# Performance work log

Measured on AMD Instinct MI355X. Metric: run time of the kernel, lower is better.

Reference implementation:

```python
import jax, jax.numpy as jnp
import numpy as np

BN_EPS = 1e-5
MIN_DIST = 1e-10


def _conv_bn_relu(x, w, b, gamma, beta):
    # pointwise Conv1d (kernel=1) == per-point linear, then BatchNorm1d (training-mode
    # batch stats, biased variance, as torch does for normalization), then ReLU.
    y = jnp.einsum('oc,bcn->bon', w, x) + b[None, :, None]
    mu = y.mean(axis=(0, 2))
    var = y.var(axis=(0, 2))
    yn = (y - mu[None, :, None]) * jax.lax.rsqrt(var + BN_EPS)[None, :, None]
    return jax.nn.relu(yn * gamma[None, :, None] + beta[None, :, None])


def setup_inputs() -> dict:
    key = jax.random.key(0)
    ks = jax.random.split(key, 12)
    B, N1, N2, C1, C2 = 8, 8192, 2048, 128, 256
    in_ch = C1 + C2  # 384
    mlp = [256, 128]
    inp = {
        'xyz1': jax.random.normal(ks[0], (B, N1, 3), jnp.float32),
        'xyz2': jax.random.normal(ks[1], (B, N2, 3), jnp.float32),
        'points1': jax.random.normal(ks[2], (B, C1, N1), jnp.float32),
        'points2': jax.random.normal(ks[3], (B, C2, N2), jnp.float32),
    }
    last = in_ch
    for i, out_ch in enumerate(mlp):
        scale = 1.0 / np.sqrt(last)
        inp[f'w{i}'] = jax.random.uniform(ks[4 + 2 * i], (out_ch, last), jnp.float32, -scale, scale)
        inp[f'b{i}'] = jax.random.uniform(ks[5 + 2 * i], (out_ch,), jnp.float32, -scale, scale)
        inp[f'gamma{i}'] = jnp.ones((out_ch,), jnp.float32)
        inp[f'beta{i}'] = jnp.zeros((out_ch,), jnp.float32)
        last = out_ch
    return inp


def reference(xyz1, xyz2, points1, points2,
              w0, b0, gamma0, beta0, w1, b1, gamma1, beta1):
    # Euclidean distance matrix [B, N1, N2] (torch.cdist, p=2)
    sq = (jnp.sum(xyz1 * xyz1, -1)[:, :, None]
          + jnp.sum(xyz2 * xyz2, -1)[:, None, :]
          - 2.0 * jnp.einsum('bnd,bmd->bnm', xyz1, xyz2))
    dists = jnp.sqrt(jnp.maximum(sq, 0.0))
    # 3 smallest distances + indices (ascending, matching torch.topk largest=False)
    neg_d, knn_idx = jax.lax.top_k(-dists, 3)  # [B, N1, 3]
    knn_d = jnp.maximum(-neg_d, MIN_DIST)
    weights = 1.0 / knn_d
    weights = weights / jnp.sum(weights, axis=2, keepdims=True)  # [B, N1, 3]
    # gather neighbor features: points2 [B, C2, N2] -> [B, C2, N1, 3]
    knn_feats = jnp.take_along_axis(points2[:, :, None, :],
                                    knn_idx[:, None, :, :], axis=3)
    interpolated = jnp.sum(knn_feats * weights[:, None, :, :], axis=3)  # [B, C2, N1]
    new_points = jnp.concatenate([points1, interpolated], axis=1)  # [B, C1+C2, N1]
    new_points = _conv_bn_relu(new_points, w0, b0, gamma0, beta0)
    new_points = _conv_bn_relu(new_points, w1, b1, gamma1, beta1)
    return new_points
```

## Files before the change

kernel.cpp:

```cpp
#include <hip/hip_runtime.h>
#include <cstdint>

using u16 = unsigned short;
typedef short bf16x8 __attribute__((ext_vector_type(8)));
typedef float f32x4 __attribute__((ext_vector_type(4)));

__device__ __forceinline__ float bf2f(u16 h) {
    union { unsigned u; float f; } x;
    x.u = ((unsigned)h) << 16;
    return x.f;
}
__device__ __forceinline__ u16 f2bf(float f) {
    union { float f; unsigned u; } x;
    x.f = f;
    unsigned r = x.u + 0x7fffu + ((x.u >> 16) & 1u);
    return (u16)(r >> 16);
}

__device__ __forceinline__ void gl_lds16(const u16* g, u16* l) {
    __builtin_amdgcn_global_load_lds((const __attribute__((address_space(1))) void*)g,
                                     (__attribute__((address_space(3))) void*)l, 16, 0, 0);
}

#define N1 8192
#define N2 2048
#define C2 256

__global__ __launch_bounds__(256) void prep_misc(const float* __restrict__ w0,
                                                 const float* __restrict__ w1,
                                                 const float* __restrict__ xyz2,
                                                 u16* __restrict__ w0b,
                                                 u16* __restrict__ w1b,
                                                 float4* __restrict__ P2P,
                                                 float* __restrict__ stats) {
    int bid = blockIdx.x, tid = threadIdx.x;
    if (bid < 384) {
        int i = bid * 256 + tid;
        w0b[i] = f2bf(w0[i]);
    } else if (bid < 512) {
        int i = (bid - 384) * 256 + tid;
        w1b[i] = f2bf(w1[i]);
    } else if (bid < 576) {
        int i = (bid - 512) * 256 + tid;
        float x = xyz2[i * 3 + 0], y = xyz2[i * 3 + 1], z = xyz2[i * 3 + 2];
        float nsq = __fadd_rn(__fadd_rn(__fmul_rn(x, x), __fmul_rn(y, y)), __fmul_rn(z, z));
        P2P[i] = make_float4(-2.0f * x, -2.0f * y, -2.0f * z, nsq);
    } else {
        for (int i = tid; i < 768; i += 256) stats[i] = 0.0f;
    }
}

__global__ __launch_bounds__(256) void transpose_to_bf16(const float* __restrict__ src,
                                                         u16* __restrict__ dst,
                                                         int C, int N, int dst_stride,
                                                         int col_off) {
    __shared__ float tile[32][33];
    int b = blockIdx.z;
    int n0 = blockIdx.x * 32, c0 = blockIdx.y * 32;
    int tx = threadIdx.x & 31, ty = threadIdx.x >> 5;
    const float* s = src + (long)b * C * N;
#pragma unroll
    for (int i = 0; i < 4; i++) {
        int c = ty + i * 8;
        tile[c][tx] = s[(long)(c0 + c) * N + n0 + tx];
    }
    __syncthreads();
    u16* d = dst + (long)b * N * dst_stride;
#pragma unroll
    for (int i = 0; i < 4; i++) {
        int n = ty + i * 8;
        d[(long)(n0 + n) * dst_stride + col_off + c0 + tx] = f2bf(tile[tx][n]);
    }
}

__global__ __launch_bounds__(512) void knn_interp(const float* __restrict__ xyz1,
                                                  const float4* __restrict__ P2P,
                                                  const u16* __restrict__ P2T,
                                                  u16* __restrict__ X) {
    __shared__ float4 pts[N2];
    __shared__ float m_d[8][64][3];
    __shared__ int   m_i[8][64][3];
    __shared__ int   s_idx[64][3];
    __shared__ float s_w[64][3];
    int b = blockIdx.y;
    int n0 = blockIdx.x * 64;
    int tid = threadIdx.x;
    int ql = tid & 63;
    int part = __builtin_amdgcn_readfirstlane(tid >> 6);

    {
        const float4* src = P2P + (long)b * N2;
        for (int j = tid; j < N2; j += 512) pts[j] = src[j];
    }

    int n = n0 + ql;
    float px = xyz1[((long)b * N1 + n) * 3 + 0];
    float py = xyz1[((long)b * N1 + n) * 3 + 1];
    float pz = xyz1[((long)b * N1 + n) * 3 + 2];
    float psq = __fadd_rn(__fadd_rn(__fmul_rn(px, px), __fmul_rn(py, py)), __fmul_rn(pz, pz));
    __syncthreads();

    const float4* lp = &pts[part * (N2 / 8)];
    int jbase = part * (N2 / 8);
    float b0 = 1e30f, b1 = 1e30f, b2 = 1e30f;
    int i0 = 0, i1 = 0, i2 = 0;
#pragma unroll 8
    for (int jj = 0; jj < N2 / 8; jj++) {
        float4 p = lp[jj];
        float u = __fadd_rn(__fadd_rn(__fmul_rn(p.x, px), __fmul_rn(p.y, py)),
                            __fmul_rn(p.z, pz));
        float sq = __fadd_rn(__fadd_rn(psq, p.w), u);
        int j = jbase + jj;
        bool c0 = sq < b0, c1 = sq < b1, c2 = sq < b2;
        i2 = c2 ? (c1 ? i1 : j) : i2;
        i1 = c1 ? (c0 ? i0 : j) : i1;
        i0 = c0 ? j : i0;
        float m1 = fmaxf(b0, sq);
        b0 = fminf(b0, sq);
        float m2 = fmaxf(b1, m1);
        b1 = fminf(b1, m1);
        b2 = fminf(b2, m2);
    }
    m_d[part][ql][0] = b0; m_d[part][ql][1] = b1; m_d[part][ql][2] = b2;
    m_i[part][ql][0] = i0; m_i[part][ql][1] = i1; m_i[part][ql][2] = i2;
    __syncthreads();

    if (tid < 64) {
        float c0 = 1e30f, c1 = 1e30f, c2 = 1e30f;
        int a0 = 0x7fffffff, a1 = 0x7fffffff, a2 = 0x7fffffff;
#pragma unroll
        for (int pp2 = 0; pp2 < 8; pp2++) {
#pragma unroll
            for (int k = 0; k < 3; k++) {
                float d = m_d[pp2][tid][k];
                int ix = m_i[pp2][tid][k];
                if (d < c2 || (d == c2 && ix < a2)) {
                    if (d < c1 || (d == c1 && ix < a1)) {
                        c2 = c1; a2 = a1;
                        if (d < c0 || (d == c0 && ix < a0)) { c1 = c0; a1 = a0; c0 = d; a0 = ix; }
                        else                                { c1 = d; a1 = ix; }
                    } else { c2 = d; a2 = ix; }
                }
            }
        }
        float e0 = sqrtf(fmaxf(c0, 0.0f));
        float e1 = sqrtf(fmaxf(c1, 0.0f));
        float e2 = sqrtf(fmaxf(c2, 0.0f));
        float kd0 = fmaxf(e0, 1e-10f), kd1 = fmaxf(e1, 1e-10f), kd2 = fmaxf(e2, 1e-10f);
        float w0 = __fdiv_rn(1.0f, kd0), w1 = __fdiv_rn(1.0f, kd1), w2 = __fdiv_rn(1.0f, kd2);
        float wsum = __fadd_rn(__fadd_rn(w0, w1), w2);
        s_idx[tid][0] = a0; s_idx[tid][1] = a1; s_idx[tid][2] = a2;
        s_w[tid][0] = __fdiv_rn(w0, wsum);
        s_w[tid][1] = __fdiv_rn(w1, wsum);
        s_w[tid][2] = __fdiv_rn(w2, wsum);
    }
    __syncthreads();

    int l = tid & 63;
    const u16* base = P2T + (long)b * N2 * C2;
    for (int p = part; p < 64; p += 8) {
        int j0 = s_idx[p][0], j1 = s_idx[p][1], j2 = s_idx[p][2];
        float f0 = s_w[p][0], f1 = s_w[p][1], f2 = s_w[p][2];
        ushort4 r0 = *(const ushort4*)&base[(long)j0 * C2 + l * 4];
        ushort4 r1 = *(const ushort4*)&base[(long)j1 * C2 + l * 4];
        ushort4 r2 = *(const ushort4*)&base[(long)j2 * C2 + l * 4];
        ushort4 o;
        o.x = f2bf(__fadd_rn(__fadd_rn(__fmul_rn(bf2f(r0.x), f0), __fmul_rn(bf2f(r1.x), f1)),
                             __fmul_rn(bf2f(r2.x), f2)));
        o.y = f2bf(__fadd_rn(__fadd_rn(__fmul_rn(bf2f(r0.y), f0), __fmul_rn(bf2f(r1.y), f1)),
                             __fmul_rn(bf2f(r2.y), f2)));
        o.z = f2bf(__fadd_rn(__fadd_rn(__fmul_rn(bf2f(r0.z), f0), __fmul_rn(bf2f(r1.z), f1)),
                             __fmul_rn(bf2f(r2.z), f2)));
        o.w = f2bf(__fadd_rn(__fadd_rn(__fmul_rn(bf2f(r0.w), f0), __fmul_rn(bf2f(r1.w), f1)),
                             __fmul_rn(bf2f(r2.w), f2)));
        *(ushort4*)&X[(long)(b * N1 + n0 + p) * 384 + 128 + l * 4] = o;
    }
}

template <int KDIM, bool BN_IN, bool ASYNC>
__global__ __launch_bounds__(256) void gemm_bn(const u16* __restrict__ A,
                                               const u16* __restrict__ Bw,
                                               const float* __restrict__ bias,
                                               const float* __restrict__ g_in_sum,
                                               const float* __restrict__ g_in_ssq,
                                               const float* __restrict__ gamma_in,
                                               const float* __restrict__ beta_in,
                                               u16* __restrict__ Yout, int Ntot,
                                               float* __restrict__ g_out_sum,
                                               float* __restrict__ g_out_ssq) {
    constexpr int LD = ASYNC ? 32 : 40;
    __shared__ __align__(16) u16 Al[128 * LD];
    __shared__ __align__(16) u16 Bl[128 * LD];
    __shared__ float s_stats[256];
    __shared__ float s_scale[BN_IN ? KDIM : 2];
    __shared__ float s_shift[BN_IN ? KDIM : 2];

    int tid = threadIdx.x;
    long s0 = (long)blockIdx.x * 128;
    int o0 = blockIdx.y * 128;

    s_stats[tid] = 0.0f;
    if constexpr (BN_IN) {
        for (int k = tid; k < KDIM; k += 256) {
            float mu = g_in_sum[k] * (1.0f / 65536.0f);
            float var = g_in_ssq[k] * (1.0f / 65536.0f) - mu * mu;
            float rs = rsqrtf(var + 1e-5f);
            float sc = gamma_in[k] * rs;
            s_scale[k] = sc;
            s_shift[k] = beta_in[k] - mu * sc;
        }
    }
    int wid = tid >> 6, lane = tid & 63;
    int wm = wid >> 1, wn = wid & 1;
    int q = lane >> 4, l16 = lane & 15;

    f32x4 acc[4][4];
#pragma unroll
    for (int mi = 0; mi < 4; mi++)
#pragma unroll
        for (int ni = 0; ni < 4; ni++) acc[mi][ni] = (f32x4){0.f, 0.f, 0.f, 0.f};

    int rbase0 = wid * 32;
    int rsub = lane >> 2;
    int colsw = (((lane & 3) ^ (rsub & 3)) << 3);
    const u16* gA0 = A + (s0 + rbase0 + rsub) * KDIM + colsw;
    const u16* gA1 = gA0 + (long)16 * KDIM;
    const u16* gB0 = Bw + (long)(o0 + rbase0 + rsub) * KDIM + colsw;
    const u16* gB1 = gB0 + (long)16 * KDIM;
    u16* lA0 = &Al[rbase0 * 32];
    u16* lA1 = &Al[(rbase0 + 16) * 32];
    u16* lB0 = &Bl[rbase0 * 32];
    u16* lB1 = &Bl[(rbase0 + 16) * 32];
    int qA = ASYNC ? (q ^ (l16 & 3)) : q;

    __syncthreads();

    for (int kt = 0; kt < KDIM; kt += 32) {
        if constexpr (ASYNC) {
            gl_lds16(gA0 + kt, lA0);
            gl_lds16(gA1 + kt, lA1);
            gl_lds16(gB0 + kt, lB0);
            gl_lds16(gB1 + kt, lB1);
        } else {
#pragma unroll
            for (int cc = 0; cc < 2; cc++) {
                int ci = tid + cc * 256;
                int row = ci >> 2;
                int kc = (ci & 3) << 3;
                union { uint4 u; u16 h[8]; } va;
                va.u = *(const uint4*)(A + (s0 + row) * KDIM + kt + kc);
                if constexpr (BN_IN) {
#pragma unroll
                    for (int j = 0; j < 8; j++) {
                        float f = bf2f(va.h[j]);
                        f = fmaxf(fmaf(f, s_scale[kt + kc + j], s_shift[kt + kc + j]), 0.0f);
                        va.h[j] = f2bf(f);
                    }
                }
                *(uint4*)&Al[row * LD + kc] = va.u;
                *(uint4*)&Bl[row * LD + kc] = *(const uint4*)(Bw + (long)(o0 + row) * KDIM + kt + kc);
            }
        }
        __syncthreads();
        bf16x8 af[4], bfr[4];
#pragma unroll
        for (int mi = 0; mi < 4; mi++)
            af[mi] = *(const bf16x8*)&Al[(wm * 64 + mi * 16 + l16) * LD + qA * 8];
#pragma unroll
        for (int ni = 0; ni < 4; ni++)
            bfr[ni] = *(const bf16x8*)&Bl[(wn * 64 + ni * 16 + l16) * LD + qA * 8];
#pragma unroll
        for (int mi = 0; mi < 4; mi++)
#pragma unroll
            for (int ni = 0; ni < 4; ni++)
                acc[mi][ni] = __builtin_amdgcn_mfma_f32_16x16x32_bf16(af[mi], bfr[ni],
                                                                      acc[mi][ni], 0, 0, 0);
        __syncthreads();
    }

#pragma unroll
    for (int ni = 0; ni < 4; ni++) {
        int coll = wn * 64 + ni * 16 + l16;
        int col = o0 + coll;
        float bz = bias[col];
        float s1 = 0.0f, s2 = 0.0f;
#pragma unroll
        for (int mi = 0; mi < 4; mi++) {
#pragma unroll
            for (int r = 0; r < 4; r++) {
                float v = acc[mi][ni][r] + bz;
                s1 += v;
                s2 += v * v;
                long row = s0 + wm * 64 + mi * 16 + q * 4 + r;
                Yout[row * Ntot + col] = f2bf(v);
            }
        }
        s1 += __shfl_xor(s1, 16, 64);
        s1 += __shfl_xor(s1, 32, 64);
        s2 += __shfl_xor(s2, 16, 64);
        s2 += __shfl_xor(s2, 32, 64);
        if (q == 0) {
            atomicAdd(&s_stats[coll], s1);
            atomicAdd(&s_stats[128 + coll], s2);
        }
    }
    __syncthreads();
    if (tid < 128) {
        atomicAdd(&g_out_sum[o0 + tid], s_stats[tid]);
        atomicAdd(&g_out_ssq[o0 + tid], s_stats[128 + tid]);
    }
}

__global__ __launch_bounds__(256) void finalize_k(const u16* __restrict__ Y1,
                                                  const float* __restrict__ g_sum,
                                                  const float* __restrict__ g_ssq,
                                                  const float* __restrict__ gamma,
                                                  const float* __restrict__ beta,
                                                  float* __restrict__ out) {
    __shared__ float s_scale[128], s_shift[128];
    int tid = threadIdx.x;
    if (tid < 128) {
        float mu = g_sum[tid] * (1.0f / 65536.0f);
        float var = g_ssq[tid] * (1.0f / 65536.0f) - mu * mu;
        float rs = rsqrtf(var + 1e-5f);
        float sc = gamma[tid] * rs;
        s_scale[tid] = sc;
        s_shift[tid] = beta[tid] - mu * sc;
    }
    __syncthreads();
    long s = (long)blockIdx.x * 256 + tid;
    int b = (int)(s >> 13);
    int n = (int)(s & 8191);
    const u16* yrow = Y1 + s * 128;
    float* obase = out + (long)b * 128 * 8192 + n;
#pragma unroll
    for (int oc = 0; oc < 128; oc += 8) {
        union { uint4 u; u16 h[8]; } va;
        va.u = *(const uint4*)&yrow[oc];
#pragma unroll
        for (int k = 0; k < 8; k++) {
            int o = oc + k;
            float v = fmaxf(fmaf(bf2f(va.h[k]), s_scale[o], s_shift[o]), 0.0f);
            obase[(long)o * 8192] = v;
        }
    }
}

extern "C" void kernel_launch(void* const* d_in, const int* in_sizes, int n_in,
                              void* d_out, int out_size, void* d_ws, size_t ws_size,
                              hipStream_t stream) {
    const float* xyz1    = (const float*)d_in[0];
    const float* xyz2    = (const float*)d_in[1];
    const float* points1 = (const float*)d_in[2];
    const float* points2 = (const float*)d_in[3];
    const float* w0 = (const float*)d_in[4];
    const float* b0 = (const float*)d_in[5];
    const float* gamma0 = (const float*)d_in[6];
    const float* beta0 = (const float*)d_in[7];
    const float* w1 = (const float*)d_in[8];
    const float* b1 = (const float*)d_in[9];
    const float* gamma1 = (const float*)d_in[10];
    const float* beta1 = (const float*)d_in[11];
    float* out = (float*)d_out;

    char* ws = (char*)d_ws;
    u16* X      = (u16*)(ws + 0);
    u16* P2T    = (u16*)(ws + 50331648);
    u16* w0b    = (u16*)(ws + 58720256);
    u16* w1b    = (u16*)(ws + 58916864);
    u16* Y0     = (u16*)(ws + 58982400);
    float4* P2P = (float4*)(ws + 92536832);
    u16* Y1b    = (u16*)(ws + 92798976);
    float* stats = (float*)(ws + 126091264);
    if (ws_size < 126094336) return;
    float* gsum0 = stats;
    float* gss0  = stats + 256;
    float* gsum1 = stats + 512;
    float* gss1  = stats + 640;

    prep_misc<<<577, 256, 0, stream>>>(w0, w1, xyz2, w0b, w1b, P2P, stats);
    transpose_to_bf16<<<dim3(256, 4, 8), 256, 0, stream>>>(points1, X, 128, 8192, 384, 0);
    transpose_to_bf16<<<dim3(64, 8, 8), 256, 0, stream>>>(points2, P2T, 256, 2048, 256, 0);
    knn_interp<<<dim3(128, 8), 512, 0, stream>>>(xyz1, P2P, P2T, X);
    gemm_bn<384, false, true><<<dim3(512, 2), 256, 0, stream>>>(
        X, w0b, b0, nullptr, nullptr, nullptr, nullptr, Y0, 256, gsum0, gss0);
    gemm_bn<256, true, false><<<dim3(512, 1), 256, 0, stream>>>(
        Y0, w1b, b1, gsum0, gss0, gamma0, beta0, Y1b, 128, gsum1, gss1);
    finalize_k<<<256, 256, 0, stream>>>(Y1b, gsum1, gss1, gamma1, beta1, out);
}
```

Before: 277.6 us.

## Compute xyz2 norms inside knn kernel and halve threads per block

Drops the P2P precompute from prep_misc, so knn_interp now loads raw xyz2 and computes squared norms into LDS itself. The block shrinks from 512 to 256 threads, so each of 4 parts scans N2/4 candidates instead of 8 parts scanning N2/8. The branchless min/max top-3 update becomes a branchy insertion. The distance formula now computes -2*dot explicitly. The intent is to cut a precompute pass and workspace traffic, at the cost of less parallelism per query and possible wave divergence in the scan.

```diff
diff --git a/kernel.cpp b/kernel.cpp
--- a/kernel.cpp
+++ b/kernel.cpp
@@ -28,10 +28,8 @@
 
 __global__ __launch_bounds__(256) void prep_misc(const float* __restrict__ w0,
                                                  const float* __restrict__ w1,
-                                                 const float* __restrict__ xyz2,
                                                  u16* __restrict__ w0b,
                                                  u16* __restrict__ w1b,
-                                                 float4* __restrict__ P2P,
                                                  float* __restrict__ stats) {
     int bid = blockIdx.x, tid = threadIdx.x;
     if (bid < 384) {
@@ -40,11 +38,6 @@
     } else if (bid < 512) {
         int i = (bid - 384) * 256 + tid;
         w1b[i] = f2bf(w1[i]);
-    } else if (bid < 576) {
-        int i = (bid - 512) * 256 + tid;
-        float x = xyz2[i * 3 + 0], y = xyz2[i * 3 + 1], z = xyz2[i * 3 + 2];
-        float nsq = __fadd_rn(__fadd_rn(__fmul_rn(x, x), __fmul_rn(y, y)), __fmul_rn(z, z));
-        P2P[i] = make_float4(-2.0f * x, -2.0f * y, -2.0f * z, nsq);
     } else {
         for (int i = tid; i < 768; i += 256) stats[i] = 0.0f;
     }
@@ -73,53 +66,53 @@
     }
 }
 
-__global__ __launch_bounds__(512) void knn_interp(const float* __restrict__ xyz1,
-                                                  const float4* __restrict__ P2P,
+__global__ __launch_bounds__(256) void knn_interp(const float* __restrict__ xyz1,
+                                                  const float* __restrict__ xyz2,
                                                   const u16* __restrict__ P2T,
                                                   u16* __restrict__ X) {
     __shared__ float4 pts[N2];
-    __shared__ float m_d[8][64][3];
-    __shared__ int   m_i[8][64][3];
+    __shared__ float m_d[4][64][3];
+    __shared__ int   m_i[4][64][3];
     __shared__ int   s_idx[64][3];
     __shared__ float s_w[64][3];
     int b = blockIdx.y;
     int n0 = blockIdx.x * 64;
     int tid = threadIdx.x;
     int ql = tid & 63;
-    int part = __builtin_amdgcn_readfirstlane(tid >> 6);
-
-    {
-        const float4* src = P2P + (long)b * N2;
-        for (int j = tid; j < N2; j += 512) pts[j] = src[j];
-    }
+    int part = tid >> 6;
+
+    for (int j = tid; j < N2; j += 256) {
+        float x = xyz2[((long)b * N2 + j) * 3 + 0];
+        float y = xyz2[((long)b * N2 + j) * 3 + 1];
+        float z = xyz2[((long)b * N2 + j) * 3 + 2];
+        float nsq = __fadd_rn(__fadd_rn(__fmul_rn(x, x), __fmul_rn(y, y)), __fmul_rn(z, z));
+        pts[j] = make_float4(x, y, z, nsq);
+    }
+    __syncthreads();
 
     int n = n0 + ql;
     float px = xyz1[((long)b * N1 + n) * 3 + 0];
     float py = xyz1[((long)b * N1 + n) * 3 + 1];
     float pz = xyz1[((long)b * N1 + n) * 3 + 2];
     float psq = __fadd_rn(__fadd_rn(__fmul_rn(px, px), __fmul_rn(py, py)), __fmul_rn(pz, pz));
-    __syncthreads();
-
-    const float4* lp = &pts[part * (N2 / 8)];
-    int jbase = part * (N2 / 8);
+
     float b0 = 1e30f, b1 = 1e30f, b2 = 1e30f;
     int i0 = 0, i1 = 0, i2 = 0;
+    int jbeg = part * (N2 / 4);
 #pragma unroll 8
-    for (int jj = 0; jj < N2 / 8; jj++) {
-        float4 p = lp[jj];
-        float u = __fadd_rn(__fadd_rn(__fmul_rn(p.x, px), __fmul_rn(p.y, py)),
-                            __fmul_rn(p.z, pz));
-        float sq = __fadd_rn(__fadd_rn(psq, p.w), u);
-        int j = jbase + jj;
-        bool c0 = sq < b0, c1 = sq < b1, c2 = sq < b2;
-        i2 = c2 ? (c1 ? i1 : j) : i2;
-        i1 = c1 ? (c0 ? i0 : j) : i1;
-        i0 = c0 ? j : i0;
-        float m1 = fmaxf(b0, sq);
-        b0 = fminf(b0, sq);
-        float m2 = fmaxf(b1, m1);
-        b1 = fminf(b1, m1);
-        b2 = fminf(b2, m2);
+    for (int jj = 0; jj < N2 / 4; jj++) {
+        int j = jbeg + jj;
+        float4 p = pts[j];
+        float dot = __fadd_rn(__fadd_rn(__fmul_rn(px, p.x), __fmul_rn(py, p.y)),
+                              __fmul_rn(pz, p.z));
+        float sq = __fsub_rn(__fadd_rn(psq, p.w), __fmul_rn(2.0f, dot));
+        if (sq < b2) {
+            if (sq < b1) {
+                b2 = b1; i2 = i1;
+                if (sq < b0) { b1 = b0; i1 = i0; b0 = sq; i0 = j; }
+                else         { b1 = sq; i1 = j; }
+            } else { b2 = sq; i2 = j; }
+        }
     }
     m_d[part][ql][0] = b0; m_d[part][ql][1] = b1; m_d[part][ql][2] = b2;
     m_i[part][ql][0] = i0; m_i[part][ql][1] = i1; m_i[part][ql][2] = i2;
@@ -129,11 +122,11 @@
         float c0 = 1e30f, c1 = 1e30f, c2 = 1e30f;
         int a0 = 0x7fffffff, a1 = 0x7fffffff, a2 = 0x7fffffff;
 #pragma unroll
-        for (int pp2 = 0; pp2 < 8; pp2++) {
+        for (int pp = 0; pp < 4; pp++) {
 #pragma unroll
             for (int k = 0; k < 3; k++) {
-                float d = m_d[pp2][tid][k];
-                int ix = m_i[pp2][tid][k];
+                float d = m_d[pp][tid][k];
+                int ix = m_i[pp][tid][k];
                 if (d < c2 || (d == c2 && ix < a2)) {
                     if (d < c1 || (d == c1 && ix < a1)) {
                         c2 = c1; a2 = a1;
@@ -158,7 +151,7 @@
 
     int l = tid & 63;
     const u16* base = P2T + (long)b * N2 * C2;
-    for (int p = part; p < 64; p += 8) {
+    for (int p = part; p < 64; p += 4) {
         int j0 = s_idx[p][0], j1 = s_idx[p][1], j2 = s_idx[p][2];
         float f0 = s_w[p][0], f1 = s_w[p][1], f2 = s_w[p][2];
         ushort4 r0 = *(const ushort4*)&base[(long)j0 * C2 + l * 4];
@@ -364,24 +357,23 @@
     float* out = (float*)d_out;
 
     char* ws = (char*)d_ws;
-    u16* X      = (u16*)(ws + 0);
-    u16* P2T    = (u16*)(ws + 50331648);
-    u16* w0b    = (u16*)(ws + 58720256);
-    u16* w1b    = (u16*)(ws + 58916864);
-    u16* Y0     = (u16*)(ws + 58982400);
-    float4* P2P = (float4*)(ws + 92536832);
-    u16* Y1b    = (u16*)(ws + 92798976);
-    float* stats = (float*)(ws + 126091264);
-    if (ws_size < 126094336) return;
+    u16* X       = (u16*)(ws + 0);
+    u16* P2T     = (u16*)(ws + 50331648);
+    u16* w0b     = (u16*)(ws + 58720256);
+    u16* w1b     = (u16*)(ws + 58916864);
+    u16* Y0      = (u16*)(ws + 58982400);
+    u16* Y1b     = (u16*)(ws + 92536832);
+    float* stats = (float*)(ws + 109314048);
+    if (ws_size < 109317120) return;
     float* gsum0 = stats;
     float* gss0  = stats + 256;
     float* gsum1 = stats + 512;
     float* gss1  = stats + 640;
 
-    prep_misc<<<577, 256, 0, stream>>>(w0, w1, xyz2, w0b, w1b, P2P, stats);
+    prep_misc<<<513, 256, 0, stream>>>(w0, w1, w0b, w1b, stats);
     transpose_to_bf16<<<dim3(256, 4, 8), 256, 0, stream>>>(points1, X, 128, 8192, 384, 0);
     transpose_to_bf16<<<dim3(64, 8, 8), 256, 0, stream>>>(points2, P2T, 256, 2048, 256, 0);
-    knn_interp<<<dim3(128, 8), 512, 0, stream>>>(xyz1, P2P, P2T, X);
+    knn_interp<<<dim3(128, 8), 256, 0, stream>>>(xyz1, xyz2, P2T, X);
     gemm_bn<384, false, true><<<dim3(512, 2), 256, 0, stream>>>(
         X, w0b, b0, nullptr, nullptr, nullptr, nullptr, Y0, 256, gsum0, gss0);
     gemm_bn<256, true, false><<<dim3(512, 1), 256, 0, stream>>>(
```

Result: faster. 268.2 us (-3.4%).
